# Kernel optimization log

Hardware: AMD Instinct MI355X
Metric: run time of the kernel (lower is better)

The kernel has to match this reference:

```python
import jax, jax.numpy as jnp
import numpy as np

# IntConv2d config
IN_C, OUT_C, K, STRIDE, PAD = 64, 128, 3, 1, 1
BATCH, H, W = 64, 56, 56


def setup_inputs() -> dict:
    key = jax.random.key(0)
    k1, k2 = jax.random.split(key, 2)
    # int8 NHWC activations (values in [-128, 127])
    x = jax.random.randint(k1, (BATCH, H, W, IN_C), -128, 128, dtype=jnp.int32).astype(jnp.int8)
    # weight layout (O, kH, kW, I) exactly as in the torch module
    weight = jax.random.randint(k2, (OUT_C, K, K, IN_C), -128, 128, dtype=jnp.int32).astype(jnp.int8)
    # module initializes bias to zeros(int8)
    bias = jnp.zeros((OUT_C,), dtype=jnp.int8)
    return {"x": x, "weight": weight, "bias": bias}


def reference(x, weight, bias):
    # int8 conv with exact int32 accumulation (what int8conv_cuda computes),
    # NHWC activations, OHWI weights -> NHWC int32 output.
    y = jax.lax.conv_general_dilated(
        x.astype(jnp.int32),
        weight.astype(jnp.int32),
        window_strides=(STRIDE, STRIDE),
        padding=((PAD, PAD), (PAD, PAD)),
        dimension_numbers=("NHWC", "OHWI", "NHWC"),
    )
    # int8 bias broadcast-added over channel dim; promotes to int32
    return y + bias.astype(jnp.int32)
```

## Files before the change

kernel.cpp:

```cpp
#include <hip/hip_runtime.h>

typedef int int4v __attribute__((ext_vector_type(4)));

#define IN_C    64
#define OUT_C   128
#define NPIX    200704
#define KTOT    576
#define N_W     73728
#define N_OUT   25690112

#define PIXB    80

__global__ __launch_bounds__(256) void pack_w_kernel(const int* __restrict__ wgt,
                                                     char* __restrict__ w8) {
    int t = blockIdx.x * 256 + threadIdx.x;
    int byte = t & 15;
    int lane = (t >> 4) & 63;
    int ntk  = t >> 10;
    int nt   = ntk & 7;
    int kt   = ntk >> 3;
    int k = kt * 64 + ((lane >> 4) << 4) + byte;
    int n = nt * 16 + (lane & 15);
    w8[t] = (char)wgt[n * KTOT + k];
}

__global__ __launch_bounds__(256, 4) void conv_halo_kernel(const int* __restrict__ x32,
                                                           const char* __restrict__ w8,
                                                           const int* __restrict__ bias,
                                                           int* __restrict__ out) {
    __shared__ char hx[100 * PIXB];

    const int tid  = threadIdx.x;
    const int lane = tid & 63;
    const int wv   = tid >> 6;
    const int l15  = lane & 15;
    const int l4   = lane >> 4;

    const int bid = blockIdx.x;
    const int n   = bid / 49;
    const int rr  = bid - n * 49;
    const int th  = rr / 7;
    const int tw  = rr - th * 7;
    const int h0  = th * 8 - 1;
    const int w0  = tw * 8 - 1;

    for (int u = tid; u < 400; u += 256) {
        int pix = u >> 2;
        int q   = u & 3;
        int hr  = pix / 10;
        int hc  = pix - hr * 10;
        int gh  = h0 + hr;
        int gw  = w0 + hc;
        int4v pk = {0, 0, 0, 0};
        if ((unsigned)gh < 56u && (unsigned)gw < 56u) {
            const int4v* src = (const int4v*)x32 + (((n * 56 + gh) * 56 + gw) << 4) + (q << 2);
            int4v a0 = src[0], a1 = src[1], a2 = src[2], a3 = src[3];
            pk.x = (a0.x & 0xff) | ((a0.y & 0xff) << 8) | ((a0.z & 0xff) << 16) | (a0.w << 24);
            pk.y = (a1.x & 0xff) | ((a1.y & 0xff) << 8) | ((a1.z & 0xff) << 16) | (a1.w << 24);
            pk.z = (a2.x & 0xff) | ((a2.y & 0xff) << 8) | ((a2.z & 0xff) << 16) | (a2.w << 24);
            pk.w = (a3.x & 0xff) | ((a3.y & 0xff) << 8) | ((a3.z & 0xff) << 16) | (a3.w << 24);
        }
        *(int4v*)(hx + pix * PIXB + (q << 4)) = pk;
    }
    __syncthreads();

    const char* aptr = hx + ((l15 >> 3) * 10 + (l15 & 7)) * PIXB + (l4 << 4);

    int4v acc[4][2];
#pragma unroll
    for (int mt = 0; mt < 4; ++mt) {
        acc[mt][0] = (int4v){0, 0, 0, 0};
        acc[mt][1] = (int4v){0, 0, 0, 0};
    }

    const char* wp = w8 + (((wv * 2) * 64 + lane) << 4);
    int4v bc0 = *(const int4v*)(wp);
    int4v bc1 = *(const int4v*)(wp + 1024);
    int toff = 0;
#pragma unroll 1
    for (int kt = 0; kt < 9; ++kt) {
        wp += 8192;
        int4v bn0 = bc0, bn1 = bc1;
        if (kt < 8) {
            bn0 = *(const int4v*)(wp);
            bn1 = *(const int4v*)(wp + 1024);
        }
#pragma unroll
        for (int mt = 0; mt < 4; ++mt) {
            int4v a = *(const int4v*)(aptr + toff + mt * 1600);
            acc[mt][0] = __builtin_amdgcn_mfma_i32_16x16x64_i8(a, bc0, acc[mt][0], 0, 0, 0);
            acc[mt][1] = __builtin_amdgcn_mfma_i32_16x16x64_i8(a, bc1, acc[mt][1], 0, 0, 0);
        }
        bc0 = bn0;
        bc1 = bn1;
        toff += 80;
        if ((kt == 2) | (kt == 5)) toff += 560;
    }

    int* obase = out + (((n * 56 + th * 8) * 56 + tw * 8) << 7);
#pragma unroll
    for (int mt = 0; mt < 4; ++mt) {
#pragma unroll
        for (int ntl = 0; ntl < 2; ++ntl) {
            int ch = wv * 32 + ntl * 16 + l15;
            int bv = bias[ch];
#pragma unroll
            for (int r = 0; r < 4; ++r) {
                int p  = mt * 16 + l4 * 4 + r;
                int pr = p >> 3, pc = p & 7;
                obase[((pr * 56 + pc) << 7) + ch] = acc[mt][ntl][r] + bv;
            }
        }
    }
}

__global__ __launch_bounds__(256) void conv_naive_kernel(const int* __restrict__ x,
                                                         const int* __restrict__ wgt,
                                                         const int* __restrict__ bias,
                                                         int* __restrict__ out) {
    int idx = blockIdx.x * 256 + threadIdx.x;
    if (idx >= N_OUT) return;
    int ch  = idx & 127;
    int pix = idx >> 7;
    int n  = pix / 3136;
    int r2 = pix - n * 3136;
    int h  = r2 / 56;
    int w  = r2 - h * 56;
    int acc = bias[ch];
    for (int kh = 0; kh < 3; ++kh) {
        int hx = h + kh - 1;
        if ((unsigned)hx >= 56u) continue;
        for (int kw = 0; kw < 3; ++kw) {
            int wx = w + kw - 1;
            if ((unsigned)wx >= 56u) continue;
            const int* xp = x + ((n * 56 + hx) * 56 + wx) * 64;
            const int* wp = wgt + ch * KTOT + (kh * 3 + kw) * 64;
            for (int ic = 0; ic < 64; ++ic) acc += xp[ic] * wp[ic];
        }
    }
    out[idx] = acc;
}

extern "C" void kernel_launch(void* const* d_in, const int* in_sizes, int n_in,
                              void* d_out, int out_size, void* d_ws, size_t ws_size,
                              hipStream_t stream) {
    const int* x    = (const int*)d_in[0];
    const int* wgt  = (const int*)d_in[1];
    const int* bias = (const int*)d_in[2];
    int* out = (int*)d_out;

    if (ws_size >= (size_t)N_W) {
        char* w8 = (char*)d_ws;
        pack_w_kernel<<<N_W / 256, 256, 0, stream>>>(wgt, w8);
        conv_halo_kernel<<<64 * 49, 256, 0, stream>>>(x, w8, bias, out);
    } else {
        conv_naive_kernel<<<(N_OUT + 255) / 256, 256, 0, stream>>>(x, wgt, bias, out);
    }
}
```

Before: 41.61 us.

## Process two images per block and swap MFMA operands for vectorized output stores

```diff
diff --git a/kernel.cpp b/kernel.cpp
--- a/kernel.cpp
+++ b/kernel.cpp
@@ -24,11 +24,11 @@
     w8[t] = (char)wgt[n * KTOT + k];
 }
 
-__global__ __launch_bounds__(256, 4) void conv_halo_kernel(const int* __restrict__ x32,
-                                                           const char* __restrict__ w8,
-                                                           const int* __restrict__ bias,
-                                                           int* __restrict__ out) {
-    __shared__ char hx[100 * PIXB];
+__global__ __launch_bounds__(256, 4) void conv_halo2_kernel(const int* __restrict__ x32,
+                                                            const char* __restrict__ w8,
+                                                            const int* __restrict__ bias,
+                                                            int* __restrict__ out) {
+    __shared__ char hx[200 * PIXB];
 
     const int tid  = threadIdx.x;
     const int lane = tid & 63;
@@ -36,24 +36,28 @@
     const int l15  = lane & 15;
     const int l4   = lane >> 4;
 
-    const int bid = blockIdx.x;
-    const int n   = bid / 49;
-    const int rr  = bid - n * 49;
-    const int th  = rr / 7;
-    const int tw  = rr - th * 7;
-    const int h0  = th * 8 - 1;
-    const int w0  = tw * 8 - 1;
+    const int bid  = blockIdx.x;
+    const int pair = bid / 49;
+    const int rr   = bid - pair * 49;
+    const int th   = rr / 7;
+    const int tw   = rr - th * 7;
+    const int n0   = pair * 2;
+    const int h0   = th * 8 - 1;
+    const int w0   = tw * 8 - 1;
 
-    for (int u = tid; u < 400; u += 256) {
+    for (int u = tid; u < 800; u += 256) {
         int pix = u >> 2;
         int q   = u & 3;
-        int hr  = pix / 10;
-        int hc  = pix - hr * 10;
+        int im  = pix >= 100;
+        int lp  = pix - im * 100;
+        int hr  = lp / 10;
+        int hc  = lp - hr * 10;
         int gh  = h0 + hr;
         int gw  = w0 + hc;
         int4v pk = {0, 0, 0, 0};
         if ((unsigned)gh < 56u && (unsigned)gw < 56u) {
-            const int4v* src = (const int4v*)x32 + (((n * 56 + gh) * 56 + gw) << 4) + (q << 2);
+            const int4v* src = (const int4v*)x32
+                             + ((((n0 + im) * 56 + gh) * 56 + gw) << 4) + (q << 2);
             int4v a0 = src[0], a1 = src[1], a2 = src[2], a3 = src[3];
             pk.x = (a0.x & 0xff) | ((a0.y & 0xff) << 8) | ((a0.z & 0xff) << 16) | (a0.w << 24);
             pk.y = (a1.x & 0xff) | ((a1.y & 0xff) << 8) | ((a1.z & 0xff) << 16) | (a1.w << 24);
@@ -66,9 +70,9 @@
 
     const char* aptr = hx + ((l15 >> 3) * 10 + (l15 & 7)) * PIXB + (l4 << 4);
 
-    int4v acc[4][2];
+    int4v acc[8][2];
 #pragma unroll
-    for (int mt = 0; mt < 4; ++mt) {
+    for (int mt = 0; mt < 8; ++mt) {
         acc[mt][0] = (int4v){0, 0, 0, 0};
         acc[mt][1] = (int4v){0, 0, 0, 0};
     }
@@ -86,10 +90,10 @@
             bn1 = *(const int4v*)(wp + 1024);
         }
 #pragma unroll
-        for (int mt = 0; mt < 4; ++mt) {
-            int4v a = *(const int4v*)(aptr + toff + mt * 1600);
-            acc[mt][0] = __builtin_amdgcn_mfma_i32_16x16x64_i8(a, bc0, acc[mt][0], 0, 0, 0);
-            acc[mt][1] = __builtin_amdgcn_mfma_i32_16x16x64_i8(a, bc1, acc[mt][1], 0, 0, 0);
+        for (int mt = 0; mt < 8; ++mt) {
+            int4v a = *(const int4v*)(aptr + toff + (mt & 3) * 1600 + (mt >> 2) * 8000);
+            acc[mt][0] = __builtin_amdgcn_mfma_i32_16x16x64_i8(bc0, a, acc[mt][0], 0, 0, 0);
+            acc[mt][1] = __builtin_amdgcn_mfma_i32_16x16x64_i8(bc1, a, acc[mt][1], 0, 0, 0);
         }
         bc0 = bn0;
         bc1 = bn1;
@@ -97,20 +101,18 @@
         if ((kt == 2) | (kt == 5)) toff += 560;
     }
 
-    int* obase = out + (((n * 56 + th * 8) * 56 + tw * 8) << 7);
+    const int chb = wv * 32 + (l4 << 2);
+    int4v bv0 = *(const int4v*)(bias + chb);
+    int4v bv1 = *(const int4v*)(bias + chb + 16);
+    int* ob0 = out + (((n0 * 56 + th * 8) * 56 + tw * 8) << 7);
+    int* ob1 = ob0 + (3136 << 7);
+    const int pc = l15 & 7;
 #pragma unroll
-    for (int mt = 0; mt < 4; ++mt) {
-#pragma unroll
-        for (int ntl = 0; ntl < 2; ++ntl) {
-            int ch = wv * 32 + ntl * 16 + l15;
-            int bv = bias[ch];
-#pragma unroll
-            for (int r = 0; r < 4; ++r) {
-                int p  = mt * 16 + l4 * 4 + r;
-                int pr = p >> 3, pc = p & 7;
-                obase[((pr * 56 + pc) << 7) + ch] = acc[mt][ntl][r] + bv;
-            }
-        }
+    for (int mt = 0; mt < 8; ++mt) {
+        int pr = ((mt & 3) << 1) + (l15 >> 3);
+        int* ob = ((mt < 4) ? ob0 : ob1) + ((pr * 56 + pc) << 7) + chb;
+        *(int4v*)(ob)      = acc[mt][0] + bv0;
+        *(int4v*)(ob + 16) = acc[mt][1] + bv1;
     }
 }
 
@@ -128,12 +130,12 @@
     int w  = r2 - h * 56;
     int acc = bias[ch];
     for (int kh = 0; kh < 3; ++kh) {
-        int hx = h + kh - 1;
-        if ((unsigned)hx >= 56u) continue;
+        int hxr = h + kh - 1;
+        if ((unsigned)hxr >= 56u) continue;
         for (int kw = 0; kw < 3; ++kw) {
             int wx = w + kw - 1;
             if ((unsigned)wx >= 56u) continue;
-            const int* xp = x + ((n * 56 + hx) * 56 + wx) * 64;
+            const int* xp = x + ((n * 56 + hxr) * 56 + wx) * 64;
             const int* wp = wgt + ch * KTOT + (kh * 3 + kw) * 64;
             for (int ic = 0; ic < 64; ++ic) acc += xp[ic] * wp[ic];
         }
@@ -152,7 +154,7 @@
     if (ws_size >= (size_t)N_W) {
         char* w8 = (char*)d_ws;
         pack_w_kernel<<<N_W / 256, 256, 0, stream>>>(wgt, w8);
-        conv_halo_kernel<<<64 * 49, 256, 0, stream>>>(x, w8, bias, out);
+        conv_halo2_kernel<<<32 * 49, 256, 0, stream>>>(x, w8, bias, out);
     } else {
         conv_naive_kernel<<<(N_OUT + 255) / 256, 256, 0, stream>>>(x, wgt, bias, out);
     }
```

After: 45.67 us. 1.1x slower.

## Swap MFMA operands for vectorized output stores, remap blocks, vectorize weight pack

Applied to the files above, without the earlier changes.

```diff
diff --git a/kernel.cpp b/kernel.cpp
--- a/kernel.cpp
+++ b/kernel.cpp
@@ -12,16 +12,19 @@
 #define PIXB    80
 
 __global__ __launch_bounds__(256) void pack_w_kernel(const int* __restrict__ wgt,
-                                                     char* __restrict__ w8) {
+                                                     unsigned int* __restrict__ w8) {
     int t = blockIdx.x * 256 + threadIdx.x;
-    int byte = t & 15;
-    int lane = (t >> 4) & 63;
-    int ntk  = t >> 10;
+    int d = t << 2;
+    int byte = d & 15;
+    int lane = (d >> 4) & 63;
+    int ntk  = d >> 10;
     int nt   = ntk & 7;
     int kt   = ntk >> 3;
     int k = kt * 64 + ((lane >> 4) << 4) + byte;
     int n = nt * 16 + (lane & 15);
-    w8[t] = (char)wgt[n * KTOT + k];
+    int4v v = *(const int4v*)(wgt + n * KTOT + k);
+    w8[t] = (v.x & 0xff) | ((v.y & 0xff) << 8) | ((v.z & 0xff) << 16)
+          | ((unsigned int)v.w << 24);
 }
 
 __global__ __launch_bounds__(256, 4) void conv_halo_kernel(const int* __restrict__ x32,
@@ -37,8 +40,10 @@
     const int l4   = lane >> 4;
 
     const int bid = blockIdx.x;
-    const int n   = bid / 49;
-    const int rr  = bid - n * 49;
+    const int nb  = (bid & 7) * 392 + (bid >> 3);
+
+    const int n   = nb / 49;
+    const int rr  = nb - n * 49;
     const int th  = rr / 7;
     const int tw  = rr - th * 7;
     const int h0  = th * 8 - 1;
@@ -80,16 +85,13 @@
 #pragma unroll 1
     for (int kt = 0; kt < 9; ++kt) {
         wp += 8192;
-        int4v bn0 = bc0, bn1 = bc1;
-        if (kt < 8) {
-            bn0 = *(const int4v*)(wp);
-            bn1 = *(const int4v*)(wp + 1024);
-        }
+        int4v bn0 = *(const int4v*)(wp);
+        int4v bn1 = *(const int4v*)(wp + 1024);
 #pragma unroll
         for (int mt = 0; mt < 4; ++mt) {
             int4v a = *(const int4v*)(aptr + toff + mt * 1600);
-            acc[mt][0] = __builtin_amdgcn_mfma_i32_16x16x64_i8(a, bc0, acc[mt][0], 0, 0, 0);
-            acc[mt][1] = __builtin_amdgcn_mfma_i32_16x16x64_i8(a, bc1, acc[mt][1], 0, 0, 0);
+            acc[mt][0] = __builtin_amdgcn_mfma_i32_16x16x64_i8(bc0, a, acc[mt][0], 0, 0, 0);
+            acc[mt][1] = __builtin_amdgcn_mfma_i32_16x16x64_i8(bc1, a, acc[mt][1], 0, 0, 0);
         }
         bc0 = bn0;
         bc1 = bn1;
@@ -97,20 +99,18 @@
         if ((kt == 2) | (kt == 5)) toff += 560;
     }
 
-    int* obase = out + (((n * 56 + th * 8) * 56 + tw * 8) << 7);
+    const int chb = wv * 32 + (l4 << 2);
+    int4v bv0 = *(const int4v*)(bias + chb);
+    int4v bv1 = *(const int4v*)(bias + chb + 16);
+    int* ob = out + (((n * 56 + th * 8) * 56 + tw * 8) << 7);
+    const int pc = l15 & 7;
+    const int prl = l15 >> 3;
 #pragma unroll
     for (int mt = 0; mt < 4; ++mt) {
-#pragma unroll
-        for (int ntl = 0; ntl < 2; ++ntl) {
-            int ch = wv * 32 + ntl * 16 + l15;
-            int bv = bias[ch];
-#pragma unroll
-            for (int r = 0; r < 4; ++r) {
-                int p  = mt * 16 + l4 * 4 + r;
-                int pr = p >> 3, pc = p & 7;
-                obase[((pr * 56 + pc) << 7) + ch] = acc[mt][ntl][r] + bv;
-            }
-        }
+        int pr = (mt << 1) + prl;
+        int* o = ob + ((pr * 56 + pc) << 7) + chb;
+        *(int4v*)(o)      = acc[mt][0] + bv0;
+        *(int4v*)(o + 16) = acc[mt][1] + bv1;
     }
 }
 
@@ -128,12 +128,12 @@
     int w  = r2 - h * 56;
     int acc = bias[ch];
     for (int kh = 0; kh < 3; ++kh) {
-        int hx = h + kh - 1;
-        if ((unsigned)hx >= 56u) continue;
+        int hxr = h + kh - 1;
+        if ((unsigned)hxr >= 56u) continue;
         for (int kw = 0; kw < 3; ++kw) {
             int wx = w + kw - 1;
             if ((unsigned)wx >= 56u) continue;
-            const int* xp = x + ((n * 56 + hx) * 56 + wx) * 64;
+            const int* xp = x + ((n * 56 + hxr) * 56 + wx) * 64;
             const int* wp = wgt + ch * KTOT + (kh * 3 + kw) * 64;
             for (int ic = 0; ic < 64; ++ic) acc += xp[ic] * wp[ic];
         }
@@ -149,10 +149,10 @@
     const int* bias = (const int*)d_in[2];
     int* out = (int*)d_out;
 
-    if (ws_size >= (size_t)N_W) {
+    if (ws_size >= (size_t)(N_W + 8192)) {
         char* w8 = (char*)d_ws;
-        pack_w_kernel<<<N_W / 256, 256, 0, stream>>>(wgt, w8);
-        conv_halo_kernel<<<64 * 49, 256, 0, stream>>>(x, w8, bias, out);
+        pack_w_kernel<<<N_W / 4 / 256, 256, 0, stream>>>(wgt, (unsigned int*)w8);
+        conv_halo_kernel<<<3136, 256, 0, stream>>>(x, w8, bias, out);
     } else {
         conv_naive_kernel<<<(N_OUT + 255) / 256, 256, 0, stream>>>(x, wgt, bias, out);
     }
```

New measurement: 41.64 us. Within noise of the previous version (+0.1%).
